# Performance work log

Hardware: AMD Instinct MI355X
Metric: run time of the kernel (lower is better)

## Reference

```python
import jax, jax.numpy as jnp
import numpy as np

N, T, C, O, K, L = 10000, 8, 16, 64, 16, 3


def setup_inputs():
    key = jax.random.key(0)
    ks = jax.random.split(key, 8)
    s = 0.05
    return dict(
        X=jax.random.normal(ks[0], (N, T, C), jnp.float32),
        As=jax.random.randint(ks[1], (L, T, N, K), 0, N, dtype=jnp.int32),
        key_out=jnp.zeros((1,), jnp.float32),
        key_states=jnp.zeros((2, 1), jnp.float32),
        conv_w=jax.random.normal(ks[2], (L, O, C), jnp.float32) * s,
        conv_b=jax.random.normal(ks[3], (L, O), jnp.float32) * s,
        W_ih=jax.random.normal(ks[4], (L, 4 * O, O), jnp.float32) * s,
        W_hh=jax.random.normal(ks[5], (L, 4 * O, O), jnp.float32) * s,
        b_ih=jax.random.normal(ks[6], (L, 4 * O), jnp.float32) * s,
        b_hh=jax.random.normal(ks[7], (L, 4 * O), jnp.float32) * s,
    )


def _lstm(seq, W_ih, W_hh, b_ih, b_hh):
    # seq: [T, N, O]; PyTorch LSTM gate order i, f, g, o; zero initial state.
    H = W_hh.shape[1]
    n = seq.shape[1]

    def step(carry, xt):
        h, c = carry
        gates = xt @ W_ih.T + h @ W_hh.T + (b_ih + b_hh)
        i, f, g, o = jnp.split(gates, 4, axis=-1)
        c = jax.nn.sigmoid(f) * c + jax.nn.sigmoid(i) * jnp.tanh(g)
        h = jax.nn.sigmoid(o) * jnp.tanh(c)
        return (h, c), h

    init = (jnp.zeros((n, H), seq.dtype), jnp.zeros((n, H), seq.dtype))
    (h, c), ys = jax.lax.scan(step, init, seq)
    return ys, h, c


def _level(x, A, conv_w, conv_b, W_ih, W_hh, b_ih, b_hh):
    # x: [N,T,C], A: [T,N,K] neighbor indices (align=1: ego-subtract)
    xt = jnp.transpose(x, (1, 0, 2))                       # [T,N,C]
    gathered = jax.vmap(lambda xtt, At: xtt[At])(xt, A)    # [T,N,K,C]
    rel = gathered - xt[:, :, None, :]                     # [T,N,K,C]
    # 1x1 conv over channel dim + bias
    feat = jnp.einsum('tnkc,oc->tnko', rel, conv_w) + conv_b  # [T,N,K,O]
    feat = feat.max(axis=2)                                # max-pool over K -> [T,N,O]
    ys, h, c = _lstm(feat, W_ih, W_hh, b_ih, b_hh)         # ys [T,N,O]
    return ys, h, c


def reference(X, As, key_out, key_states, conv_w, conv_b, W_ih, W_hh, b_ih, b_hh):
    # key_out/key_states only used by attention aggregator (type 5); unused here.
    ys, h, c = jax.vmap(_level, in_axes=(None, 0, 0, 0, 0, 0, 0, 0))(
        X, As, conv_w, conv_b, W_ih, W_hh, b_ih, b_hh)     # ys [L,T,N,O], h/c [L,N,O]
    # level_aggregate_type=1: AdaptiveMaxPool2d over the level axis = max over L
    X_out = jnp.transpose(ys.max(axis=0), (1, 0, 2))       # [N,T,O]
    state_h = h.max(axis=0)[:, None, :]                    # [N,1,O]
    state_c = c.max(axis=0)[:, None, :]                    # [N,1,O]
    return X_out, state_h, state_c
```

## Files before the change

### kernel.cpp

```cpp
#include <hip/hip_runtime.h>
#include <hip/hip_bf16.h>

#define NN 10000
#define TT 8
#define LL 3
#define NGRP 625

#define OUT_ELEMS 6400000
#define H_OFF 5120000
#define C_OFF 5760000

typedef __bf16 bf16;
typedef __attribute__((ext_vector_type(8))) __bf16 bf16x8;
typedef __attribute__((ext_vector_type(4))) float f32x4;
typedef __attribute__((ext_vector_type(16))) float f32x16;

__device__ __forceinline__ float sigf(float x) {
    return __builtin_amdgcn_rcpf(1.0f + __expf(-x));
}
__device__ __forceinline__ float tanhf_(float x) {
    return fmaf(2.0f, __builtin_amdgcn_rcpf(1.0f + __expf(-2.0f * x)), -1.0f);
}

__global__ void prep_kernel(const float* __restrict__ X,
                            const float* __restrict__ W_ih, const float* __restrict__ W_hh,
                            const float* __restrict__ b_ih, const float* __restrict__ b_hh,
                            bf16* __restrict__ wts, float* __restrict__ bias,
                            bf16* __restrict__ Xh) {
    int id = blockIdx.x * 256 + threadIdx.x;
    if (id < LL * 2 * 256 * 64) {
        int col = id & 63;
        int row = (id >> 6) & 255;
        int mat = (id >> 14) & 1;
        int l = id >> 15;
        const float* src = mat ? W_hh : W_ih;
        float w = src[(l * 256 + row) * 64 + col];
        int kh = col >> 5, nt = row >> 4, nn = row & 15, kk = col & 31;
        wts[((((l * 2 + mat) * 2 + kh) * 16 + nt) * 16 + nn) * 32 + kk] = (bf16)w;
    } else if (id < LL * 2 * 256 * 64 + LL * 256) {
        int id2 = id - LL * 2 * 256 * 64;
        bias[id2] = b_ih[id2] + b_hh[id2];
    } else if (Xh != nullptr) {
        int id3 = id - (LL * 2 * 256 * 64 + LL * 256);
        if (id3 < NN * TT) {
            const float* xr = X + (long)id3 * 16;
            f32x4 a = *(const f32x4*)xr,       b = *(const f32x4*)(xr + 4);
            f32x4 c = *(const f32x4*)(xr + 8), d = *(const f32x4*)(xr + 12);
            bf16x8 lo, hi;
#pragma unroll
            for (int j = 0; j < 4; ++j) {
                lo[j] = (bf16)a[j]; lo[4 + j] = (bf16)b[j];
                hi[j] = (bf16)c[j]; hi[4 + j] = (bf16)d[j];
            }
            bf16* xo = Xh + (long)id3 * 16;
            *(bf16x8*)xo = lo;
            *(bf16x8*)(xo + 8) = hi;
        }
    }
}

__global__ __launch_bounds__(256, 4) void fused_split3_kernel(
    const bf16* __restrict__ Xh, const int* __restrict__ As,
    const float* __restrict__ conv_w, const float* __restrict__ conv_b,
    const bf16* __restrict__ wts, const float* __restrict__ bias,
    float* __restrict__ slabs) {
    __shared__ __align__(16) bf16 featL[TT][16][72];
    __shared__ __align__(16) bf16 hlds[2][16][72];
    __shared__ __align__(16) bf16 swl[128][66];

    const int tid = threadIdx.x;
    const int l = blockIdx.x % 3;
    const int grp = blockIdx.x / 3;
    const int node0 = grp * 16;

    const int lane = tid & 63;
    const int wv = tid >> 6;
    const int c16 = lane & 15;
    const int q = lane >> 4;
    const int m = lane & 31;
    const int hh = lane >> 5;
    const int ch0 = hh * 8;
    const int nsub = m >> 4;
    const int kn = m & 15;

    bf16x8 B0, B1;
    {
        const float* w0 = conv_w + ((l * 64 + m) * 16 + ch0);
        f32x4 a = *(const f32x4*)w0, b = *(const f32x4*)(w0 + 4);
        const float* w1 = conv_w + ((l * 64 + 32 + m) * 16 + ch0);
        f32x4 c = *(const f32x4*)w1, d = *(const f32x4*)(w1 + 4);
#pragma unroll
        for (int j = 0; j < 4; ++j) {
            B0[j] = (bf16)a[j]; B0[4 + j] = (bf16)b[j];
            B1[j] = (bf16)c[j]; B1[4 + j] = (bf16)d[j];
        }
    }
    const float cb0 = conv_b[l * 64 + m];
    const float cb1 = conv_b[l * 64 + 32 + m];

    int aidx[4][4];
#pragma unroll
    for (int c = 0; c < 4; ++c) {
        const int t0 = (c >> 1) * 4;
        const int gn = node0 + 2 * (2 * wv + (c & 1)) + nsub;
#pragma unroll
        for (int j = 0; j < 4; ++j)
            aidx[c][j] = As[((long)(l * 8 + t0 + j) * NN + gn) * 16 + kn];
    }

    {
        bf16x8 ae = *(const bf16x8*)(Xh + ((long)(node0 * 8 + 32 * wv + m)) * 16 + ch0);
        f32x16 E0, E1;
#pragma unroll
        for (int k = 0; k < 16; ++k) { E0[k] = 0.0f; E1[k] = 0.0f; }
        E0 = __builtin_amdgcn_mfma_f32_32x32x16_bf16(ae, B0, E0, 0, 0, 0);
        E1 = __builtin_amdgcn_mfma_f32_32x32x16_bf16(ae, B1, E1, 0, 0, 0);
#pragma unroll
        for (int g = 0; g < 16; ++g) {
            const int r = (g & 3) + 8 * (g >> 2) + 4 * hh;
            swl[32 * wv + r][m]      = (bf16)E0[g];
            swl[32 * wv + r][32 + m] = (bf16)E1[g];
        }
    }

    bf16x8 gA[4], gB[4];
    auto gload = [&](int c, bf16x8* dst) {
        const int t0 = (c >> 1) * 4;
#pragma unroll
        for (int j = 0; j < 4; ++j)
            dst[j] = *(const bf16x8*)(Xh + ((long)aidx[c][j] * 8 + t0 + j) * 16 + ch0);
    };
    auto proc = [&](int c, const bf16x8* g) {
        const int t0 = (c >> 1) * 4;
        const int pc = 2 * wv + (c & 1);
        const int rowb = 32 * wv + (2 * (c & 1) + hh) * 8 + t0;
#pragma unroll
        for (int j = 0; j < 4; ++j) {
            f32x16 D0, D1;
#pragma unroll
            for (int k = 0; k < 16; ++k) { D0[k] = 0.0f; D1[k] = 0.0f; }
            D0 = __builtin_amdgcn_mfma_f32_32x32x16_bf16(g[j], B0, D0, 0, 0, 0);
            D1 = __builtin_amdgcn_mfma_f32_32x32x16_bf16(g[j], B1, D1, 0, 0, 0);

            float v00 = D0[0], v01 = D1[0], v10 = D0[8], v11 = D1[8];
#pragma unroll
            for (int k = 1; k < 8; ++k) {
                v00 = fmaxf(v00, D0[k]);     v01 = fmaxf(v01, D1[k]);
                v10 = fmaxf(v10, D0[8 + k]); v11 = fmaxf(v11, D1[8 + k]);
            }
            v00 = fmaxf(v00, __shfl_xor(v00, 32));
            v01 = fmaxf(v01, __shfl_xor(v01, 32));
            v10 = fmaxf(v10, __shfl_xor(v10, 32));
            v11 = fmaxf(v11, __shfl_xor(v11, 32));

            const float sA = hh ? v10 : v00;
            const float sB = hh ? v11 : v01;
            const float swA = (float)swl[rowb + j][m];
            const float swB = (float)swl[rowb + j][32 + m];
            featL[t0 + j][2 * pc + hh][m]      = (bf16)(sA + cb0 - swA);
            featL[t0 + j][2 * pc + hh][32 + m] = (bf16)(sB + cb1 - swB);
        }
    };
    gload(0, gA); gload(1, gB);
    proc(0, gA);  gload(2, gA);
    proc(1, gB);  gload(3, gB);
    proc(2, gA);
    proc(3, gB);

    const bf16* wb = wts + l * 32768;
    const int fo = c16 * 32 + q * 8;
    bf16x8 Bx0[4], Bx1[4], Bh0[4], Bh1[4];
    float brg[4];
#pragma unroll
    for (int g = 0; g < 4; ++g) {
        const int nt = 4 * g + wv;
        Bx0[g] = *(const bf16x8*)(wb + (0 * 16 + nt) * 512 + fo);
        Bx1[g] = *(const bf16x8*)(wb + (1 * 16 + nt) * 512 + fo);
        Bh0[g] = *(const bf16x8*)(wb + (2 * 16 + nt) * 512 + fo);
        Bh1[g] = *(const bf16x8*)(wb + (3 * 16 + nt) * 512 + fo);
        brg[g] = bias[l * 256 + nt * 16 + c16];
    }
    float c_r[4];
#pragma unroll
    for (int r = 0; r < 4; ++r) c_r[r] = 0.0f;

    float* slab = slabs + (long)l * OUT_ELEMS;
    const int col = wv * 16 + c16;

#pragma unroll
    for (int t = 0; t < TT; ++t) {
        __syncthreads();

        bf16x8 ax0 = *(const bf16x8*)&featL[t][c16][q * 8];
        bf16x8 ax1 = *(const bf16x8*)&featL[t][c16][32 + q * 8];
        bf16x8 ah0, ah1;
        if (t > 0) {
            ah0 = *(const bf16x8*)&hlds[(t + 1) & 1][c16][q * 8];
            ah1 = *(const bf16x8*)&hlds[(t + 1) & 1][c16][32 + q * 8];
        }

        f32x4 acc[4];
#pragma unroll
        for (int g = 0; g < 4; ++g) {
            float b = brg[g];
            acc[g] = (f32x4){b, b, b, b};
            acc[g] = __builtin_amdgcn_mfma_f32_16x16x32_bf16(ax0, Bx0[g], acc[g], 0, 0, 0);
            acc[g] = __builtin_amdgcn_mfma_f32_16x16x32_bf16(ax1, Bx1[g], acc[g], 0, 0, 0);
            if (t > 0) {
                acc[g] = __builtin_amdgcn_mfma_f32_16x16x32_bf16(ah0, Bh0[g], acc[g], 0, 0, 0);
                acc[g] = __builtin_amdgcn_mfma_f32_16x16x32_bf16(ah1, Bh1[g], acc[g], 0, 0, 0);
            }
        }

#pragma unroll
        for (int r = 0; r < 4; ++r) {
            float iv = acc[0][r], fv = acc[1][r], gg = acc[2][r], ov = acc[3][r];
            float c = sigf(fv) * c_r[r] + sigf(iv) * tanhf_(gg);
            c_r[r] = c;
            float h = sigf(ov) * tanhf_(c);
            hlds[t & 1][q * 4 + r][col] = (bf16)h;
            slab[((long)(node0 + q * 4 + r) * 8 + t) * 64 + col] = h;
            if (t == TT - 1) {
                slab[H_OFF + (long)(node0 + q * 4 + r) * 64 + col] = h;
                slab[C_OFF + (long)(node0 + q * 4 + r) * 64 + col] = c;
            }
        }
    }
}

__global__ __launch_bounds__(256) void reduce_kernel(
    const float* __restrict__ slabs, float* __restrict__ out) {
    const long i = (long)blockIdx.x * 256 + threadIdx.x;
    const f32x4* s0 = (const f32x4*)slabs;
    const f32x4* s1 = (const f32x4*)(slabs + OUT_ELEMS);
    const f32x4* s2 = (const f32x4*)(slabs + 2L * OUT_ELEMS);
    f32x4 a = s0[i], b = s1[i], c = s2[i], d;
#pragma unroll
    for (int k = 0; k < 4; ++k) d[k] = fmaxf(fmaxf(a[k], b[k]), c[k]);
    ((f32x4*)out)[i] = d;
}

__device__ __forceinline__ void level_body(
    int l, int node0, int tid,
    const float* __restrict__ X, const int* __restrict__ As,
    const float* __restrict__ conv_w, const float* __restrict__ conv_b,
    const bf16* __restrict__ wts, const float* __restrict__ bias,
    bf16 (*featL)[16][72], bf16 (*hlds)[16][72],
    float ymax[TT][4], float hfin[4], float cfin[4], bool accum) {
    const int lane = tid & 63;
    const int wv = tid >> 6;
    const int c16 = lane & 15;
    const int q = lane >> 4;
    const int m = lane & 31;
    const int hh = lane >> 5;
    const int ch0 = hh * 8;
    const int nsub = m >> 4;
    const int kn = m & 15;

    bf16x8 B0, B1;
    {
        const float* w0 = conv_w + ((l * 64 + m) * 16 + ch0);
        f32x4 a = *(const f32x4*)w0, b = *(const f32x4*)(w0 + 4);
        const float* w1 = conv_w + ((l * 64 + 32 + m) * 16 + ch0);
        f32x4 c = *(const f32x4*)w1, d = *(const f32x4*)(w1 + 4);
#pragma unroll
        for (int j = 0; j < 4; ++j) {
            B0[j] = (bf16)a[j]; B0[4 + j] = (bf16)b[j];
            B1[j] = (bf16)c[j]; B1[4 + j] = (bf16)d[j];
        }
    }
    const float cb0 = conv_b[l * 64 + m];
    const float cb1 = conv_b[l * 64 + 32 + m];

#pragma unroll 1
    for (int c = 0; c < 4; ++c) {
        const int pc = 2 * wv + (c & 1);
        const int t0 = (c >> 1) * 4;
        const int gn = node0 + 2 * pc + nsub;

        int aidx[4];
#pragma unroll
        for (int j = 0; j < 4; ++j)
            aidx[j] = As[((long)(l * 8 + t0 + j) * NN + gn) * 16 + kn];
        f32x4 sv[4][2], gv[4][2];
#pragma unroll
        for (int j = 0; j < 4; ++j) {
            const float* sp = X + ((gn * 8 + t0 + j) * 16 + ch0);
            sv[j][0] = *(const f32x4*)sp;
            sv[j][1] = *(const f32x4*)(sp + 4);
        }
#pragma unroll
        for (int j = 0; j < 4; ++j) {
            const float* gp = X + (((long)aidx[j] * 8 + t0 + j) * 16 + ch0);
            gv[j][0] = *(const f32x4*)gp;
            gv[j][1] = *(const f32x4*)(gp + 4);
        }

#pragma unroll
        for (int j = 0; j < 4; ++j) {
            bf16x8 af;
#pragma unroll
            for (int k = 0; k < 4; ++k) {
                af[k]     = (bf16)(gv[j][0][k] - sv[j][0][k]);
                af[4 + k] = (bf16)(gv[j][1][k] - sv[j][1][k]);
            }
            f32x16 D0, D1;
#pragma unroll
            for (int k = 0; k < 16; ++k) { D0[k] = 0.0f; D1[k] = 0.0f; }
            D0 = __builtin_amdgcn_mfma_f32_32x32x16_bf16(af, B0, D0, 0, 0, 0);
            D1 = __builtin_amdgcn_mfma_f32_32x32x16_bf16(af, B1, D1, 0, 0, 0);

            float v00 = D0[0], v01 = D1[0], v10 = D0[8], v11 = D1[8];
#pragma unroll
            for (int k = 1; k < 8; ++k) {
                v00 = fmaxf(v00, D0[k]);     v01 = fmaxf(v01, D1[k]);
                v10 = fmaxf(v10, D0[8 + k]); v11 = fmaxf(v11, D1[8 + k]);
            }
            v00 = fmaxf(v00, __shfl_xor(v00, 32));
            v01 = fmaxf(v01, __shfl_xor(v01, 32));
            v10 = fmaxf(v10, __shfl_xor(v10, 32));
            v11 = fmaxf(v11, __shfl_xor(v11, 32));

            const float sA = hh ? v10 : v00;
            const float sB = hh ? v11 : v01;
            featL[t0 + j][2 * pc + hh][m]      = (bf16)(sA + cb0);
            featL[t0 + j][2 * pc + hh][32 + m] = (bf16)(sB + cb1);
        }
    }

    const bf16* wb = wts + l * 32768;
    const int fo = c16 * 32 + q * 8;
    bf16x8 Bx0[4], Bx1[4], Bh0[4], Bh1[4];
    float brg[4];
#pragma unroll
    for (int g = 0; g < 4; ++g) {
        const int nt = 4 * g + wv;
        Bx0[g] = *(const bf16x8*)(wb + (0 * 16 + nt) * 512 + fo);
        Bx1[g] = *(const bf16x8*)(wb + (1 * 16 + nt) * 512 + fo);
        Bh0[g] = *(const bf16x8*)(wb + (2 * 16 + nt) * 512 + fo);
        Bh1[g] = *(const bf16x8*)(wb + (3 * 16 + nt) * 512 + fo);
        brg[g] = bias[l * 256 + nt * 16 + c16];
    }
    float c_r[4];
#pragma unroll
    for (int r = 0; r < 4; ++r) c_r[r] = 0.0f;

#pragma unroll
    for (int t = 0; t < TT; ++t) {
        __syncthreads();

        bf16x8 ax0 = *(const bf16x8*)&featL[t][c16][q * 8];
        bf16x8 ax1 = *(const bf16x8*)&featL[t][c16][32 + q * 8];
        bf16x8 ah0, ah1;
        if (t > 0) {
            ah0 = *(const bf16x8*)&hlds[(t + 1) & 1][c16][q * 8];
            ah1 = *(const bf16x8*)&hlds[(t + 1) & 1][c16][32 + q * 8];
        }

        f32x4 acc[4];
#pragma unroll
        for (int g = 0; g < 4; ++g) {
            float b = brg[g];
            acc[g] = (f32x4){b, b, b, b};
            acc[g] = __builtin_amdgcn_mfma_f32_16x16x32_bf16(ax0, Bx0[g], acc[g], 0, 0, 0);
            acc[g] = __builtin_amdgcn_mfma_f32_16x16x32_bf16(ax1, Bx1[g], acc[g], 0, 0, 0);
            if (t > 0) {
                acc[g] = __builtin_amdgcn_mfma_f32_16x16x32_bf16(ah0, Bh0[g], acc[g], 0, 0, 0);
                acc[g] = __builtin_amdgcn_mfma_f32_16x16x32_bf16(ah1, Bh1[g], acc[g], 0, 0, 0);
            }
        }

#pragma unroll
        for (int r = 0; r < 4; ++r) {
            float iv = acc[0][r], fv = acc[1][r], gg = acc[2][r], ov = acc[3][r];
            float c = sigf(fv) * c_r[r] + sigf(iv) * tanhf_(gg);
            c_r[r] = c;
            float h = sigf(ov) * tanhf_(c);
            hlds[t & 1][q * 4 + r][wv * 16 + c16] = (bf16)h;
            ymax[t][r] = accum ? fmaxf(ymax[t][r], h) : h;
            if (t == TT - 1) {
                hfin[r] = accum ? fmaxf(hfin[r], h) : h;
                cfin[r] = accum ? fmaxf(cfin[r], c) : c;
            }
        }
    }
}

__global__ __launch_bounds__(256, 3) void fused_kernel(
    const float* __restrict__ X, const int* __restrict__ As,
    const float* __restrict__ conv_w, const float* __restrict__ conv_b,
    const bf16* __restrict__ wts, const float* __restrict__ bias,
    float* __restrict__ out) {
    __shared__ __align__(16) bf16 featL[TT][16][72];
    __shared__ __align__(16) bf16 hlds[2][16][72];

    const int tid = threadIdx.x;
    const int node0 = blockIdx.x * 16;

    float ymax[TT][4], hfin[4], cfin[4];
    for (int l = 0; l < LL; ++l) {
        __syncthreads();
        level_body(l, node0, tid, X, As, conv_w, conv_b, wts, bias,
                   featL, hlds, ymax, hfin, cfin, (l > 0));
    }

    const int lane = tid & 63;
    const int wv = tid >> 6;
    const int c16 = lane & 15;
    const int q = lane >> 4;
    const int col = wv * 16 + c16;
#pragma unroll
    for (int t = 0; t < TT; ++t)
#pragma unroll
        for (int r = 0; r < 4; ++r)
            out[((long)(node0 + q * 4 + r) * 8 + t) * 64 + col] = ymax[t][r];
    float* sh = out + (long)H_OFF;
    float* sc = out + (long)C_OFF;
#pragma unroll
    for (int r = 0; r < 4; ++r) {
        sh[(long)(node0 + q * 4 + r) * 64 + col] = hfin[r];
        sc[(long)(node0 + q * 4 + r) * 64 + col] = cfin[r];
    }
}

extern "C" void kernel_launch(void* const* d_in, const int* in_sizes, int n_in,
                              void* d_out, int out_size, void* d_ws, size_t ws_size,
                              hipStream_t stream) {
    const float* X = (const float*)d_in[0];
    const int* As = (const int*)d_in[1];
    const float* conv_w = (const float*)d_in[4];
    const float* conv_b = (const float*)d_in[5];
    const float* W_ih = (const float*)d_in[6];
    const float* W_hh = (const float*)d_in[7];
    const float* b_ih = (const float*)d_in[8];
    const float* b_hh = (const float*)d_in[9];
    float* out = (float*)d_out;

    char* ws = (char*)d_ws;
    const size_t slabs_bytes = (size_t)3 * OUT_ELEMS * 4;
    const size_t xh_bytes = (size_t)NN * TT * 16 * 2;
    const size_t need = slabs_bytes + 196608 + 4096 + xh_bytes;
    const bool big_ws = ws_size >= need;

    if (big_ws) {
        float* slabs = (float*)ws;
        bf16* wts = (bf16*)(ws + slabs_bytes);
        float* bias = (float*)(ws + slabs_bytes + 196608);
        bf16* Xh = (bf16*)(ws + slabs_bytes + 196608 + 4096);
        hipLaunchKernelGGL(prep_kernel, dim3(700), dim3(256), 0, stream,
                           X, W_ih, W_hh, b_ih, b_hh, wts, bias, Xh);
        hipLaunchKernelGGL(fused_split3_kernel, dim3(3 * NGRP), dim3(256), 0, stream,
                           Xh, As, conv_w, conv_b, wts, bias, slabs);
        hipLaunchKernelGGL(reduce_kernel, dim3(OUT_ELEMS / 4 / 256), dim3(256), 0, stream,
                           slabs, out);
    } else {
        bf16* wts = (bf16*)ws;
        float* bias = (float*)(ws + 196608);
        hipLaunchKernelGGL(prep_kernel, dim3(700), dim3(256), 0, stream,
                           X, W_ih, W_hh, b_ih, b_hh, wts, bias, (bf16*)nullptr);
        hipLaunchKernelGGL(fused_kernel, dim3(NGRP), dim3(256), 0, stream,
                           X, As, conv_w, conv_b, wts, bias, out);
    }
}
```

Baseline: 181.8 us.

## Fuse three per-level blocks and level-max reduction into one 768-thread kernel

Replaces the per-level split kernel plus separate reduce kernel with a single kernel where each 768-thread block handles all three levels for 16 nodes, doing the max over levels in shared memory and writing the final output directly. This removes the large fp32 slab buffer round-trip through global memory and one kernel launch. The ego-term correction is now exchanged through register shuffles instead of a shared-memory table. In exchange, occupancy falls to one large block per launch slot, with extra syncs and cross-level coupling inside a block.

```diff
diff --git a/kernel.cpp b/kernel.cpp
--- a/kernel.cpp
+++ b/kernel.cpp
@@ -59,22 +59,21 @@
     }
 }
 
-__global__ __launch_bounds__(256, 4) void fused_split3_kernel(
+__global__ __launch_bounds__(768, 1) void mega_kernel(
     const bf16* __restrict__ Xh, const int* __restrict__ As,
     const float* __restrict__ conv_w, const float* __restrict__ conv_b,
     const bf16* __restrict__ wts, const float* __restrict__ bias,
-    float* __restrict__ slabs) {
-    __shared__ __align__(16) bf16 featL[TT][16][72];
-    __shared__ __align__(16) bf16 hlds[2][16][72];
-    __shared__ __align__(16) bf16 swl[128][66];
+    float* __restrict__ out) {
+    __shared__ __align__(16) bf16 featL[LL][TT][16][72];
+    __shared__ __align__(16) bf16 hlds[LL][2][16][72];
+    __shared__ __align__(16) float yst[LL][2][16][64];
 
     const int tid = threadIdx.x;
-    const int l = blockIdx.x % 3;
-    const int grp = blockIdx.x / 3;
-    const int node0 = grp * 16;
-
+    const int node0 = blockIdx.x * 16;
+    const int lq = tid >> 8;
+    const int tl = tid & 255;
     const int lane = tid & 63;
-    const int wv = tid >> 6;
+    const int wq = tl >> 6;
     const int c16 = lane & 15;
     const int q = lane >> 4;
     const int m = lane & 31;
@@ -85,9 +84,9 @@
 
     bf16x8 B0, B1;
     {
-        const float* w0 = conv_w + ((l * 64 + m) * 16 + ch0);
+        const float* w0 = conv_w + ((lq * 64 + m) * 16 + ch0);
         f32x4 a = *(const f32x4*)w0, b = *(const f32x4*)(w0 + 4);
-        const float* w1 = conv_w + ((l * 64 + 32 + m) * 16 + ch0);
+        const float* w1 = conv_w + ((lq * 64 + 32 + m) * 16 + ch0);
         f32x4 c = *(const f32x4*)w1, d = *(const f32x4*)(w1 + 4);
 #pragma unroll
         for (int j = 0; j < 4; ++j) {
@@ -95,32 +94,26 @@
             B1[j] = (bf16)c[j]; B1[4 + j] = (bf16)d[j];
         }
     }
-    const float cb0 = conv_b[l * 64 + m];
-    const float cb1 = conv_b[l * 64 + 32 + m];
+    const float cb0 = conv_b[lq * 64 + m];
+    const float cb1 = conv_b[lq * 64 + 32 + m];
 
     int aidx[4][4];
 #pragma unroll
     for (int c = 0; c < 4; ++c) {
         const int t0 = (c >> 1) * 4;
-        const int gn = node0 + 2 * (2 * wv + (c & 1)) + nsub;
+        const int gn = node0 + 2 * (2 * wq + (c & 1)) + nsub;
 #pragma unroll
         for (int j = 0; j < 4; ++j)
-            aidx[c][j] = As[((long)(l * 8 + t0 + j) * NN + gn) * 16 + kn];
-    }
-
+            aidx[c][j] = As[((long)(lq * 8 + t0 + j) * NN + gn) * 16 + kn];
+    }
+
+    f32x16 E0, E1;
     {
-        bf16x8 ae = *(const bf16x8*)(Xh + ((long)(node0 * 8 + 32 * wv + m)) * 16 + ch0);
-        f32x16 E0, E1;
+        bf16x8 ae = *(const bf16x8*)(Xh + ((long)(node0 * 8 + 32 * wq + m)) * 16 + ch0);
 #pragma unroll
         for (int k = 0; k < 16; ++k) { E0[k] = 0.0f; E1[k] = 0.0f; }
         E0 = __builtin_amdgcn_mfma_f32_32x32x16_bf16(ae, B0, E0, 0, 0, 0);
         E1 = __builtin_amdgcn_mfma_f32_32x32x16_bf16(ae, B1, E1, 0, 0, 0);
-#pragma unroll
-        for (int g = 0; g < 16; ++g) {
-            const int r = (g & 3) + 8 * (g >> 2) + 4 * hh;
-            swl[32 * wv + r][m]      = (bf16)E0[g];
-            swl[32 * wv + r][32 + m] = (bf16)E1[g];
-        }
     }
 
     bf16x8 gA[4], gB[4];
@@ -132,8 +125,7 @@
     };
     auto proc = [&](int c, const bf16x8* g) {
         const int t0 = (c >> 1) * 4;
-        const int pc = 2 * wv + (c & 1);
-        const int rowb = 32 * wv + (2 * (c & 1) + hh) * 8 + t0;
+        const int pc = 2 * wq + (c & 1);
 #pragma unroll
         for (int j = 0; j < 4; ++j) {
             f32x16 D0, D1;
@@ -155,10 +147,21 @@
 
             const float sA = hh ? v10 : v00;
             const float sB = hh ? v11 : v01;
-            const float swA = (float)swl[rowb + j][m];
-            const float swB = (float)swl[rowb + j][32 + m];
-            featL[t0 + j][2 * pc + hh][m]      = (bf16)(sA + cb0 - swA);
-            featL[t0 + j][2 * pc + hh][32 + m] = (bf16)(sB + cb1 - swB);
+
+            const float a0 = E0[j + 8 * (c & 1)];
+            const float a1 = E0[j + 8 * (c & 1) + 4];
+            const float b0 = E1[j + 8 * (c & 1)];
+            const float b1 = E1[j + 8 * (c & 1) + 4];
+            const float sendA = hh ? a0 : a1;
+            const float sendB = hh ? b0 : b1;
+            const float rcvA = __shfl_xor(sendA, 32);
+            const float rcvB = __shfl_xor(sendB, 32);
+            const bool loc = (hh == (c >> 1));
+            const float swA = loc ? (hh ? a1 : a0) : rcvA;
+            const float swB = loc ? (hh ? b1 : b0) : rcvB;
+
+            featL[lq][t0 + j][2 * pc + hh][m]      = (bf16)(sA + cb0 - swA);
+            featL[lq][t0 + j][2 * pc + hh][32 + m] = (bf16)(sB + cb1 - swB);
         }
     };
     gload(0, gA); gload(1, gB);
@@ -167,36 +170,47 @@
     proc(2, gA);
     proc(3, gB);
 
-    const bf16* wb = wts + l * 32768;
+    const bf16* wb = wts + lq * 32768;
     const int fo = c16 * 32 + q * 8;
     bf16x8 Bx0[4], Bx1[4], Bh0[4], Bh1[4];
     float brg[4];
 #pragma unroll
     for (int g = 0; g < 4; ++g) {
-        const int nt = 4 * g + wv;
+        const int nt = 4 * g + wq;
         Bx0[g] = *(const bf16x8*)(wb + (0 * 16 + nt) * 512 + fo);
         Bx1[g] = *(const bf16x8*)(wb + (1 * 16 + nt) * 512 + fo);
         Bh0[g] = *(const bf16x8*)(wb + (2 * 16 + nt) * 512 + fo);
         Bh1[g] = *(const bf16x8*)(wb + (3 * 16 + nt) * 512 + fo);
-        brg[g] = bias[l * 256 + nt * 16 + c16];
+        brg[g] = bias[lq * 256 + nt * 16 + c16];
     }
     float c_r[4];
 #pragma unroll
     for (int r = 0; r < 4; ++r) c_r[r] = 0.0f;
 
-    float* slab = slabs + (long)l * OUT_ELEMS;
-    const int col = wv * 16 + c16;
+    const int col = wq * 16 + c16;
+    const int sn = tl >> 4;
+    const int sc = (tl & 15) * 4;
 
 #pragma unroll
     for (int t = 0; t < TT; ++t) {
         __syncthreads();
 
-        bf16x8 ax0 = *(const bf16x8*)&featL[t][c16][q * 8];
-        bf16x8 ax1 = *(const bf16x8*)&featL[t][c16][32 + q * 8];
+        if (t > 0 && tid < 256) {
+            f32x4 y0 = *(const f32x4*)&yst[0][(t - 1) & 1][sn][sc];
+            f32x4 y1 = *(const f32x4*)&yst[1][(t - 1) & 1][sn][sc];
+            f32x4 y2 = *(const f32x4*)&yst[2][(t - 1) & 1][sn][sc];
+            f32x4 dmx;
+#pragma unroll
+            for (int k = 0; k < 4; ++k) dmx[k] = fmaxf(fmaxf(y0[k], y1[k]), y2[k]);
+            *(f32x4*)&out[((long)(node0 + sn) * 8 + (t - 1)) * 64 + sc] = dmx;
+        }
+
+        bf16x8 ax0 = *(const bf16x8*)&featL[lq][t][c16][q * 8];
+        bf16x8 ax1 = *(const bf16x8*)&featL[lq][t][c16][32 + q * 8];
         bf16x8 ah0, ah1;
         if (t > 0) {
-            ah0 = *(const bf16x8*)&hlds[(t + 1) & 1][c16][q * 8];
-            ah1 = *(const bf16x8*)&hlds[(t + 1) & 1][c16][32 + q * 8];
+            ah0 = *(const bf16x8*)&hlds[lq][(t + 1) & 1][c16][q * 8];
+            ah1 = *(const bf16x8*)&hlds[lq][(t + 1) & 1][c16][32 + q * 8];
         }
 
         f32x4 acc[4];
@@ -218,26 +232,35 @@
             float c = sigf(fv) * c_r[r] + sigf(iv) * tanhf_(gg);
             c_r[r] = c;
             float h = sigf(ov) * tanhf_(c);
-            hlds[t & 1][q * 4 + r][col] = (bf16)h;
-            slab[((long)(node0 + q * 4 + r) * 8 + t) * 64 + col] = h;
-            if (t == TT - 1) {
-                slab[H_OFF + (long)(node0 + q * 4 + r) * 64 + col] = h;
-                slab[C_OFF + (long)(node0 + q * 4 + r) * 64 + col] = c;
-            }
-        }
-    }
-}
-
-__global__ __launch_bounds__(256) void reduce_kernel(
-    const float* __restrict__ slabs, float* __restrict__ out) {
-    const long i = (long)blockIdx.x * 256 + threadIdx.x;
-    const f32x4* s0 = (const f32x4*)slabs;
-    const f32x4* s1 = (const f32x4*)(slabs + OUT_ELEMS);
-    const f32x4* s2 = (const f32x4*)(slabs + 2L * OUT_ELEMS);
-    f32x4 a = s0[i], b = s1[i], c = s2[i], d;
-#pragma unroll
-    for (int k = 0; k < 4; ++k) d[k] = fmaxf(fmaxf(a[k], b[k]), c[k]);
-    ((f32x4*)out)[i] = d;
+            hlds[lq][t & 1][q * 4 + r][col] = (bf16)h;
+            yst[lq][t & 1][q * 4 + r][col] = h;
+        }
+    }
+
+    __syncthreads();
+#pragma unroll
+    for (int r = 0; r < 4; ++r)
+        yst[lq][0][q * 4 + r][col] = c_r[r];
+    if (tid < 256) {
+        f32x4 y0 = *(const f32x4*)&yst[0][1][sn][sc];
+        f32x4 y1 = *(const f32x4*)&yst[1][1][sn][sc];
+        f32x4 y2 = *(const f32x4*)&yst[2][1][sn][sc];
+        f32x4 dmx;
+#pragma unroll
+        for (int k = 0; k < 4; ++k) dmx[k] = fmaxf(fmaxf(y0[k], y1[k]), y2[k]);
+        *(f32x4*)&out[((long)(node0 + sn) * 8 + 7) * 64 + sc] = dmx;
+        *(f32x4*)&out[H_OFF + (long)(node0 + sn) * 64 + sc] = dmx;
+    }
+    __syncthreads();
+    if (tid < 256) {
+        f32x4 c0 = *(const f32x4*)&yst[0][0][sn][sc];
+        f32x4 c1 = *(const f32x4*)&yst[1][0][sn][sc];
+        f32x4 c2 = *(const f32x4*)&yst[2][0][sn][sc];
+        f32x4 dmx;
+#pragma unroll
+        for (int k = 0; k < 4; ++k) dmx[k] = fmaxf(fmaxf(c0[k], c1[k]), c2[k]);
+        *(f32x4*)&out[C_OFF + (long)(node0 + sn) * 64 + sc] = dmx;
+    }
 }
 
 __device__ __forceinline__ void level_body(
@@ -437,22 +460,18 @@
     float* out = (float*)d_out;
 
     char* ws = (char*)d_ws;
-    const size_t slabs_bytes = (size_t)3 * OUT_ELEMS * 4;
     const size_t xh_bytes = (size_t)NN * TT * 16 * 2;
-    const size_t need = slabs_bytes + 196608 + 4096 + xh_bytes;
+    const size_t need = 196608 + 4096 + xh_bytes;
     const bool big_ws = ws_size >= need;
 
     if (big_ws) {
-        float* slabs = (float*)ws;
-        bf16* wts = (bf16*)(ws + slabs_bytes);
-        float* bias = (float*)(ws + slabs_bytes + 196608);
-        bf16* Xh = (bf16*)(ws + slabs_bytes + 196608 + 4096);
+        bf16* wts = (bf16*)ws;
+        float* bias = (float*)(ws + 196608);
+        bf16* Xh = (bf16*)(ws + 196608 + 4096);
         hipLaunchKernelGGL(prep_kernel, dim3(700), dim3(256), 0, stream,
                            X, W_ih, W_hh, b_ih, b_hh, wts, bias, Xh);
-        hipLaunchKernelGGL(fused_split3_kernel, dim3(3 * NGRP), dim3(256), 0, stream,
-                           Xh, As, conv_w, conv_b, wts, bias, slabs);
-        hipLaunchKernelGGL(reduce_kernel, dim3(OUT_ELEMS / 4 / 256), dim3(256), 0, stream,
-                           slabs, out);
+        hipLaunchKernelGGL(mega_kernel, dim3(NGRP), dim3(768), 0, stream,
+                           Xh, As, conv_w, conv_b, wts, bias, out);
     } else {
         bf16* wts = (bf16*)ws;
         float* bias = (float*)(ws + 196608);
```

Measured after the change: 149.8 us. -17.6%, faster.

## Replace per-level slabs and reduce kernel with atomic float max into output

Applied to the files above, without the earlier changes.

Removes the three per-level output slabs and the separate reduce kernel. The prep kernel now fills the output with -1e30, and each level's LSTM kernel combines its h/c values into the output with sign-aware integer atomicMax/atomicMin. This avoids writing and re-reading three full-size slabs and one kernel launch, at the cost of global atomics on every output element. It also drops the shared-memory staging of the ego (self) conv term and passes those values between lanes with shuffles instead, which cuts LDS usage. The launch-bounds occupancy hint drops from 4 to 3 blocks per CU.

```diff
diff --git a/kernel.cpp b/kernel.cpp
--- a/kernel.cpp
+++ b/kernel.cpp
@@ -22,11 +22,16 @@
     return fmaf(2.0f, __builtin_amdgcn_rcpf(1.0f + __expf(-2.0f * x)), -1.0f);
 }
 
+__device__ __forceinline__ void afmax(float* p, float v) {
+    if (v >= 0.0f) atomicMax((int*)p, __float_as_int(v));
+    else           atomicMin((unsigned int*)p, __float_as_uint(v));
+}
+
 __global__ void prep_kernel(const float* __restrict__ X,
                             const float* __restrict__ W_ih, const float* __restrict__ W_hh,
                             const float* __restrict__ b_ih, const float* __restrict__ b_hh,
                             bf16* __restrict__ wts, float* __restrict__ bias,
-                            bf16* __restrict__ Xh) {
+                            bf16* __restrict__ Xh, float* __restrict__ out_init) {
     int id = blockIdx.x * 256 + threadIdx.x;
     if (id < LL * 2 * 256 * 64) {
         int col = id & 63;
@@ -40,9 +45,9 @@
     } else if (id < LL * 2 * 256 * 64 + LL * 256) {
         int id2 = id - LL * 2 * 256 * 64;
         bias[id2] = b_ih[id2] + b_hh[id2];
-    } else if (Xh != nullptr) {
-        int id3 = id - (LL * 2 * 256 * 64 + LL * 256);
-        if (id3 < NN * TT) {
+    } else if (id < LL * 2 * 256 * 64 + LL * 256 + NN * TT) {
+        if (Xh != nullptr) {
+            int id3 = id - (LL * 2 * 256 * 64 + LL * 256);
             const float* xr = X + (long)id3 * 16;
             f32x4 a = *(const f32x4*)xr,       b = *(const f32x4*)(xr + 4);
             f32x4 c = *(const f32x4*)(xr + 8), d = *(const f32x4*)(xr + 12);
@@ -56,17 +61,22 @@
             *(bf16x8*)xo = lo;
             *(bf16x8*)(xo + 8) = hi;
         }
-    }
-}
-
-__global__ __launch_bounds__(256, 4) void fused_split3_kernel(
+    } else if (out_init != nullptr) {
+        long id4 = (long)id - (LL * 2 * 256 * 64 + LL * 256 + NN * TT);
+        if (id4 < OUT_ELEMS / 4) {
+            const f32x4 neg = {-1e30f, -1e30f, -1e30f, -1e30f};
+            ((f32x4*)out_init)[id4] = neg;
+        }
+    }
+}
+
+__global__ __launch_bounds__(256, 3) void fused_split4_kernel(
     const bf16* __restrict__ Xh, const int* __restrict__ As,
     const float* __restrict__ conv_w, const float* __restrict__ conv_b,
     const bf16* __restrict__ wts, const float* __restrict__ bias,
-    float* __restrict__ slabs) {
+    float* __restrict__ out) {
     __shared__ __align__(16) bf16 featL[TT][16][72];
     __shared__ __align__(16) bf16 hlds[2][16][72];
-    __shared__ __align__(16) bf16 swl[128][66];
 
     const int tid = threadIdx.x;
     const int l = blockIdx.x % 3;
@@ -108,19 +118,13 @@
             aidx[c][j] = As[((long)(l * 8 + t0 + j) * NN + gn) * 16 + kn];
     }
 
+    f32x16 E0, E1;
     {
         bf16x8 ae = *(const bf16x8*)(Xh + ((long)(node0 * 8 + 32 * wv + m)) * 16 + ch0);
-        f32x16 E0, E1;
 #pragma unroll
         for (int k = 0; k < 16; ++k) { E0[k] = 0.0f; E1[k] = 0.0f; }
         E0 = __builtin_amdgcn_mfma_f32_32x32x16_bf16(ae, B0, E0, 0, 0, 0);
         E1 = __builtin_amdgcn_mfma_f32_32x32x16_bf16(ae, B1, E1, 0, 0, 0);
-#pragma unroll
-        for (int g = 0; g < 16; ++g) {
-            const int r = (g & 3) + 8 * (g >> 2) + 4 * hh;
-            swl[32 * wv + r][m]      = (bf16)E0[g];
-            swl[32 * wv + r][32 + m] = (bf16)E1[g];
-        }
     }
 
     bf16x8 gA[4], gB[4];
@@ -133,7 +137,6 @@
     auto proc = [&](int c, const bf16x8* g) {
         const int t0 = (c >> 1) * 4;
         const int pc = 2 * wv + (c & 1);
-        const int rowb = 32 * wv + (2 * (c & 1) + hh) * 8 + t0;
 #pragma unroll
         for (int j = 0; j < 4; ++j) {
             f32x16 D0, D1;
@@ -155,8 +158,19 @@
 
             const float sA = hh ? v10 : v00;
             const float sB = hh ? v11 : v01;
-            const float swA = (float)swl[rowb + j][m];
-            const float swB = (float)swl[rowb + j][32 + m];
+
+            const float a0 = E0[j + 8 * (c & 1)];
+            const float a1 = E0[j + 8 * (c & 1) + 4];
+            const float b0 = E1[j + 8 * (c & 1)];
+            const float b1 = E1[j + 8 * (c & 1) + 4];
+            const float sendA = hh ? a0 : a1;
+            const float sendB = hh ? b0 : b1;
+            const float rcvA = __shfl_xor(sendA, 32);
+            const float rcvB = __shfl_xor(sendB, 32);
+            const bool loc = (hh == (c >> 1));
+            const float swA = loc ? (hh ? a1 : a0) : rcvA;
+            const float swB = loc ? (hh ? b1 : b0) : rcvB;
+
             featL[t0 + j][2 * pc + hh][m]      = (bf16)(sA + cb0 - swA);
             featL[t0 + j][2 * pc + hh][32 + m] = (bf16)(sB + cb1 - swB);
         }
@@ -184,7 +198,6 @@
 #pragma unroll
     for (int r = 0; r < 4; ++r) c_r[r] = 0.0f;
 
-    float* slab = slabs + (long)l * OUT_ELEMS;
     const int col = wv * 16 + c16;
 
 #pragma unroll
@@ -219,25 +232,13 @@
             c_r[r] = c;
             float h = sigf(ov) * tanhf_(c);
             hlds[t & 1][q * 4 + r][col] = (bf16)h;
-            slab[((long)(node0 + q * 4 + r) * 8 + t) * 64 + col] = h;
+            afmax(&out[((long)(node0 + q * 4 + r) * 8 + t) * 64 + col], h);
             if (t == TT - 1) {
-                slab[H_OFF + (long)(node0 + q * 4 + r) * 64 + col] = h;
-                slab[C_OFF + (long)(node0 + q * 4 + r) * 64 + col] = c;
-            }
-        }
-    }
-}
-
-__global__ __launch_bounds__(256) void reduce_kernel(
-    const float* __restrict__ slabs, float* __restrict__ out) {
-    const long i = (long)blockIdx.x * 256 + threadIdx.x;
-    const f32x4* s0 = (const f32x4*)slabs;
-    const f32x4* s1 = (const f32x4*)(slabs + OUT_ELEMS);
-    const f32x4* s2 = (const f32x4*)(slabs + 2L * OUT_ELEMS);
-    f32x4 a = s0[i], b = s1[i], c = s2[i], d;
-#pragma unroll
-    for (int k = 0; k < 4; ++k) d[k] = fmaxf(fmaxf(a[k], b[k]), c[k]);
-    ((f32x4*)out)[i] = d;
+                afmax(&out[H_OFF + (long)(node0 + q * 4 + r) * 64 + col], h);
+                afmax(&out[C_OFF + (long)(node0 + q * 4 + r) * 64 + col], c);
+            }
+        }
+    }
 }
 
 __device__ __forceinline__ void level_body(
@@ -437,27 +438,24 @@
     float* out = (float*)d_out;
 
     char* ws = (char*)d_ws;
-    const size_t slabs_bytes = (size_t)3 * OUT_ELEMS * 4;
     const size_t xh_bytes = (size_t)NN * TT * 16 * 2;
-    const size_t need = slabs_bytes + 196608 + 4096 + xh_bytes;
+    const size_t need = 196608 + 4096 + xh_bytes;
     const bool big_ws = ws_size >= need;
 
     if (big_ws) {
-        float* slabs = (float*)ws;
-        bf16* wts = (bf16*)(ws + slabs_bytes);
-        float* bias = (float*)(ws + slabs_bytes + 196608);
-        bf16* Xh = (bf16*)(ws + slabs_bytes + 196608 + 4096);
-        hipLaunchKernelGGL(prep_kernel, dim3(700), dim3(256), 0, stream,
-                           X, W_ih, W_hh, b_ih, b_hh, wts, bias, Xh);
-        hipLaunchKernelGGL(fused_split3_kernel, dim3(3 * NGRP), dim3(256), 0, stream,
-                           Xh, As, conv_w, conv_b, wts, bias, slabs);
-        hipLaunchKernelGGL(reduce_kernel, dim3(OUT_ELEMS / 4 / 256), dim3(256), 0, stream,
-                           slabs, out);
+        bf16* wts = (bf16*)ws;
+        float* bias = (float*)(ws + 196608);
+        bf16* Xh = (bf16*)(ws + 196608 + 4096);
+        hipLaunchKernelGGL(prep_kernel, dim3(6950), dim3(256), 0, stream,
+                           X, W_ih, W_hh, b_ih, b_hh, wts, bias, Xh, out);
+        hipLaunchKernelGGL(fused_split4_kernel, dim3(3 * NGRP), dim3(256), 0, stream,
+                           Xh, As, conv_w, conv_b, wts, bias, out);
     } else {
         bf16* wts = (bf16*)ws;
         float* bias = (float*)(ws + 196608);
         hipLaunchKernelGGL(prep_kernel, dim3(700), dim3(256), 0, stream,
-                           X, W_ih, W_hh, b_ih, b_hh, wts, bias, (bf16*)nullptr);
+                           X, W_ih, W_hh, b_ih, b_hh, wts, bias,
+                           (bf16*)nullptr, (float*)nullptr);
         hipLaunchKernelGGL(fused_kernel, dim3(NGRP), dim3(256), 0, stream,
                            X, As, conv_w, conv_b, wts, bias, out);
     }
```

After: 191.7 us. 5.4% more time.
